# Optimization experiments

Measured on AMD Instinct MI355X. Metric: run time of the kernel, lower is better.

The kernel has to match this reference:

```python
import jax, jax.numpy as jnp
import numpy as np

B, S, D = 8, 2048, 1024  # batch, seq_len, emb_dim == qkv_dim
NEG = -999999.0  # module uses -999999 instead of -inf


def setup_inputs() -> dict:
    key = jax.random.key(0)
    ks = jax.random.split(key, 4)
    inputs = jax.random.normal(ks[0], (B, S, D), dtype=jnp.float32)
    # causal mask, flax attention layout [B, 1, S, S]
    causal = jnp.tril(jnp.ones((S, S), dtype=bool))
    mask = jnp.broadcast_to(causal, (B, 1, S, S))
    scale = 1.0 / np.sqrt(D)
    Wq = jax.random.normal(ks[1], (D, D), dtype=jnp.float32) * scale
    Wk = jax.random.normal(ks[2], (D, D), dtype=jnp.float32) * scale
    Wv = jax.random.normal(ks[3], (D, D), dtype=jnp.float32) * scale
    z = jnp.zeros((D,), dtype=jnp.float32)
    return {"inputs": inputs, "mask": mask, "Wq": Wq, "bq": z, "Wk": Wk,
            "bk": z, "Wv": Wv, "bv": z}


def reference(inputs, mask, Wq, bq, Wk, bk, Wv, bv):
    q = inputs @ Wq + bq  # [B,S,D]
    k = inputs @ Wk + bk
    v = inputs @ Wv + bv
    depth = q.shape[-1]
    q = q / jnp.sqrt(jnp.asarray(depth, q.dtype))
    attn = jnp.einsum('bqd,bkd->bqk', q, k)  # [B,S,S]
    attn = jnp.where(jnp.squeeze(mask, axis=1), attn, NEG)
    attn = jax.nn.softmax(attn, axis=-1)
    return attn @ v  # [B,S,D]
```

## Files before the change

kernel.cpp:

```cpp
#include <hip/hip_runtime.h>
#include <hip/hip_bf16.h>
#include <cstdint>

#define S_LEN 2048
#define D_DIM 1024
#define NB 8

typedef __attribute__((ext_vector_type(8))) short bf16x8;
typedef __attribute__((ext_vector_type(4))) float f32x4;

__device__ __forceinline__ unsigned short f2bf(float f) {
  union { float f; unsigned u; } x; x.f = f;
  unsigned r = x.u + 0x7fffu + ((x.u >> 16) & 1u);
  return (unsigned short)(r >> 16);
}
__device__ __forceinline__ void gload16(const void* g, void* l) {
  __builtin_amdgcn_global_load_lds((const __attribute__((address_space(1))) void*)g,
                                   (__attribute__((address_space(3))) void*)l, 16, 0, 0);
}

__global__ __launch_bounds__(256)
void cvt_f32_bf16(const float* __restrict__ in, unsigned short* __restrict__ out, int n4) {
  int i = blockIdx.x * blockDim.x + threadIdx.x;
  if (i >= n4) return;
  float4 v = reinterpret_cast<const float4*>(in)[i];
  ushort4 o;
  o.x = f2bf(v.x); o.y = f2bf(v.y); o.z = f2bf(v.z); o.w = f2bf(v.w);
  reinterpret_cast<ushort4*>(out)[i] = o;
}

__global__ __launch_bounds__(256)
void transpose_f32_bf16(const float* __restrict__ in, unsigned short* __restrict__ out,
                        int rows, int cols) {
  __shared__ unsigned short tile[32][33];
  int bx = blockIdx.x * 32, by = blockIdx.y * 32;
  int tx = threadIdx.x, ty = threadIdx.y;
  #pragma unroll
  for (int i = ty; i < 32; i += 8)
    tile[i][tx] = f2bf(in[(size_t)(by + i) * cols + bx + tx]);
  __syncthreads();
  #pragma unroll
  for (int i = ty; i < 32; i += 8)
    out[(size_t)(bx + i) * rows + by + tx] = tile[tx][i];
}

__global__ __launch_bounds__(256)
void transpose_bf16(const unsigned short* __restrict__ in, unsigned short* __restrict__ out,
                    int ldin, int ldout, long zin, long zout) {
  __shared__ unsigned short tile[32][33];
  const unsigned short* ip = in + (size_t)blockIdx.z * zin;
  unsigned short* op = out + (size_t)blockIdx.z * zout;
  int bx = blockIdx.x * 32, by = blockIdx.y * 32;
  int tx = threadIdx.x, ty = threadIdx.y;
  #pragma unroll
  for (int i = ty; i < 32; i += 8)
    tile[i][tx] = ip[(size_t)(by + i) * ldin + bx + tx];
  __syncthreads();
  #pragma unroll
  for (int i = ty; i < 32; i += 8)
    op[(size_t)(bx + i) * ldout + by + tx] = tile[tx][i];
}

template<int MODE>
__global__ __launch_bounds__(512, 2)
void gemm8(const unsigned short* __restrict__ Aall, const unsigned short* __restrict__ Btall,
           void* __restrict__ Call, int Kd, int lda, int ldb, int ldc,
           long sAz, long sBz, long sCz,
           const float* __restrict__ b0, const float* __restrict__ b1,
           const float* __restrict__ b2, float* __restrict__ rowsum, int ntn) {
  __shared__ __align__(16) unsigned short As[2][2][8192];
  __shared__ __align__(16) unsigned short Bs[2][2][8192];
  int nwg = gridDim.x, bid = blockIdx.x;
  int wg = (bid & 7) * (nwg >> 3) + (bid >> 3);
  int tm = wg / ntn, tn = wg % ntn;
  int z = blockIdx.z;
  if (MODE == 1 && tn > tm) return;
  const unsigned short* A  = Aall  + (size_t)z * sAz;
  const unsigned short* Bt = Btall + (size_t)z * sBz;
  int m0 = tm * 256, n0 = tn * 256;
  int t = threadIdx.x, lane = t & 63, w = t >> 6;
  int wr = w >> 2, wc = w & 3;
  int lr = lane & 15, lq = lane >> 4;
  int nkt = (MODE == 2) ? (tm + 1) * 4 : (Kd >> 6);

  int offA[8], offB[4];
  #pragma unroll
  for (int mi = 0; mi < 8; ++mi) {
    int row = wr * 128 + mi * 16 + lr;
    offA[mi] = row * 32 + ((lq ^ ((row >> 1) & 3)) * 8);
  }
  #pragma unroll
  for (int ni = 0; ni < 4; ++ni) {
    int row = wc * 64 + ni * 16 + lr;
    offB[ni] = row * 32 + ((lq ^ ((row >> 1) & 3)) * 8);
  }
  int srow[2], soff[2];
  #pragma unroll
  for (int c = 0; c < 2; ++c) {
    int r = c * 128 + w * 16 + (lane >> 2);
    srow[c] = r;
    soff[c] = ((lane & 3) ^ ((r >> 1) & 3)) * 8;
  }

  f32x4 acc[8][4];
  f32x4 zero4 = {0.f, 0.f, 0.f, 0.f};
  #pragma unroll
  for (int mi = 0; mi < 8; ++mi)
    #pragma unroll
    for (int ni = 0; ni < 4; ++ni) acc[mi][ni] = zero4;

  auto stgA = [&](int buf, int kh, int kt) {
    int kb = kt * 64 + kh * 32;
    #pragma unroll
    for (int c = 0; c < 2; ++c)
      gload16(A + (size_t)(m0 + srow[c]) * lda + kb + soff[c],
              &As[buf][kh][c * 4096 + w * 512]);
  };
  auto stgB = [&](int buf, int kh, int kt) {
    int kb = kt * 64 + kh * 32;
    #pragma unroll
    for (int c = 0; c < 2; ++c)
      gload16(Bt + (size_t)(n0 + srow[c]) * ldb + kb + soff[c],
              &Bs[buf][kh][c * 4096 + w * 512]);
  };

  stgA(0, 0, 0); stgB(0, 0, 0); stgA(0, 1, 0); stgB(0, 1, 0);

  int cur = 0;
  for (int kt = 0; kt < nkt; ++kt) {
    bool pf = (kt + 1 < nkt);
    #pragma unroll
    for (int ph = 0; ph < 4; ++ph) {
      const int kk = ph >> 1, mh = ph & 1;
      if (pf || ph < 2) asm volatile("s_waitcnt vmcnt(4)" ::: "memory");
      else              asm volatile("s_waitcnt vmcnt(0)" ::: "memory");
      __builtin_amdgcn_s_barrier();
      __builtin_amdgcn_sched_barrier(0);
      bf16x8 af[4], bfv[4];
      #pragma unroll
      for (int i = 0; i < 4; ++i)
        af[i] = *reinterpret_cast<const bf16x8*>(&As[cur][kk][offA[mh * 4 + i]]);
      #pragma unroll
      for (int i = 0; i < 4; ++i)
        bfv[i] = *reinterpret_cast<const bf16x8*>(&Bs[cur][kk][offB[i]]);
      if (pf) {
        if (ph == 0)      stgA(cur ^ 1, 0, kt + 1);
        else if (ph == 1) stgB(cur ^ 1, 0, kt + 1);
        else if (ph == 2) stgA(cur ^ 1, 1, kt + 1);
        else              stgB(cur ^ 1, 1, kt + 1);
      }
      asm volatile("s_waitcnt lgkmcnt(0)" ::: "memory");
      __builtin_amdgcn_sched_barrier(0);
      __builtin_amdgcn_s_setprio(1);
      #pragma unroll
      for (int i = 0; i < 4; ++i)
        #pragma unroll
        for (int j = 0; j < 4; ++j)
          acc[mh * 4 + i][j] =
              __builtin_amdgcn_mfma_f32_16x16x32_bf16(af[i], bfv[j], acc[mh * 4 + i][j], 0, 0, 0);
      __builtin_amdgcn_s_setprio(0);
    }
    cur ^= 1;
  }

  if (MODE == 0) {
    unsigned short* C = (unsigned short*)Call;
    #pragma unroll
    for (int ni = 0; ni < 4; ++ni) {
      int col = n0 + wc * 64 + ni * 16 + lr;
      float bb, sc;
      if (col < 1024)      { bb = b0[col];        sc = 0.03125f; }
      else if (col < 2048) { bb = b1[col - 1024]; sc = 1.0f; }
      else                 { bb = b2[col - 2048]; sc = 1.0f; }
      #pragma unroll
      for (int mi = 0; mi < 8; ++mi)
        #pragma unroll
        for (int j = 0; j < 4; ++j) {
          int row = m0 + wr * 128 + mi * 16 + lq * 4 + j;
          C[(size_t)row * ldc + col] = f2bf((acc[mi][ni][j] + bb) * sc);
        }
    }
  } else if (MODE == 1) {
    unsigned short* C = (unsigned short*)Call + (size_t)z * sCz;
    float* rs = rowsum + z * S_LEN;
    #pragma unroll
    for (int mi = 0; mi < 8; ++mi)
      #pragma unroll
      for (int j = 0; j < 4; ++j) {
        int row = m0 + wr * 128 + mi * 16 + lq * 4 + j;
        float partial = 0.f;
        #pragma unroll
        for (int ni = 0; ni < 4; ++ni) {
          int col = n0 + wc * 64 + ni * 16 + lr;
          float e = (col <= row) ? __expf(acc[mi][ni][j]) : 0.f;
          partial += e;
          C[(size_t)row * ldc + col] = f2bf(e);
        }
        #pragma unroll
        for (int off = 1; off < 16; off <<= 1) partial += __shfl_xor(partial, off);
        if (lr == 0) atomicAdd(&rs[row], partial);
      }
  } else {
    float* C = (float*)Call + (size_t)z * sCz;
    const float* rs = rowsum + z * S_LEN;
    #pragma unroll
    for (int mi = 0; mi < 8; ++mi)
      #pragma unroll
      for (int j = 0; j < 4; ++j) {
        int row = m0 + wr * 128 + mi * 16 + lq * 4 + j;
        float inv = 1.f / rs[row];
        #pragma unroll
        for (int ni = 0; ni < 4; ++ni) {
          int col = n0 + wc * 64 + ni * 16 + lr;
          C[(size_t)row * ldc + col] = acc[mi][ni][j] * inv;
        }
      }
  }
}

extern "C" void kernel_launch(void* const* d_in, const int* in_sizes, int n_in,
                              void* d_out, int out_size, void* d_ws, size_t ws_size,
                              hipStream_t stream) {
  (void)in_sizes; (void)n_in; (void)out_size; (void)ws_size;
  const float* X  = (const float*)d_in[0];
  const float* Wq = (const float*)d_in[2];
  const float* bq = (const float*)d_in[3];
  const float* Wk = (const float*)d_in[4];
  const float* bk = (const float*)d_in[5];
  const float* Wv = (const float*)d_in[6];
  const float* bv = (const float*)d_in[7];

  char* ws = (char*)d_ws;
  unsigned short* Xb  = (unsigned short*)(ws);
  unsigned short* Wt  = (unsigned short*)(ws + 33554432L);
  float*          Rs  = (float*)(ws + 33554432L);
  unsigned short* QKV = (unsigned short*)(ws + 39845888L);
  unsigned short* Pb  = (unsigned short*)(ws + 140509184L);
  unsigned short* Vt  = Xb;

  cvt_f32_bf16<<<16384, 256, 0, stream>>>(X, Xb, (NB * S_LEN * D_DIM) / 4);
  dim3 tb(32, 8);
  transpose_f32_bf16<<<dim3(32, 32), tb, 0, stream>>>(Wq, Wt + 0L * 1048576L, D_DIM, D_DIM);
  transpose_f32_bf16<<<dim3(32, 32), tb, 0, stream>>>(Wk, Wt + 1L * 1048576L, D_DIM, D_DIM);
  transpose_f32_bf16<<<dim3(32, 32), tb, 0, stream>>>(Wv, Wt + 2L * 1048576L, D_DIM, D_DIM);
  gemm8<0><<<dim3(64 * 12, 1, 1), 512, 0, stream>>>(Xb, Wt, (void*)QKV,
      D_DIM, D_DIM, D_DIM, 3 * D_DIM,
      0L, 0L, 0L, bq, bk, bv, nullptr, 12);
  hipMemsetAsync(Rs, 0, NB * S_LEN * sizeof(float), stream);
  gemm8<1><<<dim3(64, 1, NB), 512, 0, stream>>>(QKV, QKV + 1024, (void*)Pb,
      D_DIM, 3 * D_DIM, 3 * D_DIM, S_LEN,
      (long)S_LEN * 3 * D_DIM, (long)S_LEN * 3 * D_DIM, (long)S_LEN * S_LEN,
      nullptr, nullptr, nullptr, Rs, 8);
  transpose_bf16<<<dim3(32, 64, NB), tb, 0, stream>>>(QKV + 2048, Vt,
      3 * D_DIM, S_LEN, (long)S_LEN * 3 * D_DIM, (long)D_DIM * S_LEN);
  gemm8<2><<<dim3(32, 1, NB), 512, 0, stream>>>(Pb, Vt, d_out,
      S_LEN, S_LEN, S_LEN, D_DIM,
      (long)S_LEN * S_LEN, (long)D_DIM * S_LEN, (long)S_LEN * D_DIM,
      nullptr, nullptr, nullptr, Rs, 4);
}
```

Before: 328.7 us.

## Use 4-stage LDS ring with register double-buffered fragments and staged bf16 stores

```diff
diff --git a/kernel.cpp b/kernel.cpp
--- a/kernel.cpp
+++ b/kernel.cpp
@@ -61,6 +61,20 @@
     op[(size_t)(bx + i) * ldout + by + tx] = tile[tx][i];
 }
 
+#define LDFRAG(S, BUF, MH)                                                        \
+  { _Pragma("unroll") for (int i_ = 0; i_ < 4; ++i_)                              \
+      af##S[i_] = *reinterpret_cast<const bf16x8*>(&As[BUF][offA[(MH)*4+i_]]);    \
+    _Pragma("unroll") for (int i_ = 0; i_ < 4; ++i_)                              \
+      bf##S[i_] = *reinterpret_cast<const bf16x8*>(&Bs[BUF][offB[i_]]); }
+
+#define DOMFMA(S, MH)                                                             \
+  { __builtin_amdgcn_s_setprio(1);                                                \
+    _Pragma("unroll") for (int i_ = 0; i_ < 4; ++i_)                              \
+      _Pragma("unroll") for (int j_ = 0; j_ < 4; ++j_)                            \
+        acc[(MH)*4+i_][j_] = __builtin_amdgcn_mfma_f32_16x16x32_bf16(             \
+            af##S[i_], bf##S[j_], acc[(MH)*4+i_][j_], 0, 0, 0);                   \
+    __builtin_amdgcn_s_setprio(0); }
+
 template<int MODE>
 __global__ __launch_bounds__(512, 2)
 void gemm8(const unsigned short* __restrict__ Aall, const unsigned short* __restrict__ Btall,
@@ -68,8 +82,8 @@
            long sAz, long sBz, long sCz,
            const float* __restrict__ b0, const float* __restrict__ b1,
            const float* __restrict__ b2, float* __restrict__ rowsum, int ntn) {
-  __shared__ __align__(16) unsigned short As[2][2][8192];
-  __shared__ __align__(16) unsigned short Bs[2][2][8192];
+  __shared__ __align__(16) unsigned short As[4][8192];
+  __shared__ __align__(16) unsigned short Bs[4][8192];
   int nwg = gridDim.x, bid = blockIdx.x;
   int wg = (bid & 7) * (nwg >> 3) + (bid >> 3);
   int tm = wg / ntn, tn = wg % ntn;
@@ -81,7 +95,7 @@
   int t = threadIdx.x, lane = t & 63, w = t >> 6;
   int wr = w >> 2, wc = w & 3;
   int lr = lane & 15, lq = lane >> 4;
-  int nkt = (MODE == 2) ? (tm + 1) * 4 : (Kd >> 6);
+  int nkt = (MODE == 2) ? (tm + 1) * 8 : (Kd >> 5);
 
   int offA[8], offB[4];
   #pragma unroll
@@ -109,97 +123,120 @@
     #pragma unroll
     for (int ni = 0; ni < 4; ++ni) acc[mi][ni] = zero4;
 
-  auto stgA = [&](int buf, int kh, int kt) {
-    int kb = kt * 64 + kh * 32;
+  auto stgA = [&](int buf, int kt2) {
+    int kb = kt2 * 32;
     #pragma unroll
     for (int c = 0; c < 2; ++c)
-      gload16(A + (size_t)(m0 + srow[c]) * lda + kb + soff[c],
-              &As[buf][kh][c * 4096 + w * 512]);
+      gload16(A + (size_t)(m0 + srow[c]) * lda + kb + soff[c], &As[buf][c * 4096 + w * 512]);
   };
-  auto stgB = [&](int buf, int kh, int kt) {
-    int kb = kt * 64 + kh * 32;
+  auto stgB = [&](int buf, int kt2) {
+    int kb = kt2 * 32;
     #pragma unroll
     for (int c = 0; c < 2; ++c)
-      gload16(Bt + (size_t)(n0 + srow[c]) * ldb + kb + soff[c],
-              &Bs[buf][kh][c * 4096 + w * 512]);
+      gload16(Bt + (size_t)(n0 + srow[c]) * ldb + kb + soff[c], &Bs[buf][c * 4096 + w * 512]);
   };
 
-  stgA(0, 0, 0); stgB(0, 0, 0); stgA(0, 1, 0); stgB(0, 1, 0);
-
-  int cur = 0;
+  stgA(0, 0); stgB(0, 0); stgA(1, 1); stgB(1, 1); stgA(2, 2); stgB(2, 2);
+  asm volatile("s_waitcnt vmcnt(8)" ::: "memory");
+  __builtin_amdgcn_s_barrier();
+  __builtin_amdgcn_sched_barrier(0);
+  bf16x8 af0[4], bf0[4], af1[4], bf1[4];
+  LDFRAG(0, 0, 0);
+
   for (int kt = 0; kt < nkt; ++kt) {
-    bool pf = (kt + 1 < nkt);
-    #pragma unroll
-    for (int ph = 0; ph < 4; ++ph) {
-      const int kk = ph >> 1, mh = ph & 1;
-      if (pf || ph < 2) asm volatile("s_waitcnt vmcnt(4)" ::: "memory");
-      else              asm volatile("s_waitcnt vmcnt(0)" ::: "memory");
+    int bcur = kt & 3, bpre = (kt + 3) & 3, bnxt = (kt + 1) & 3;
+    bool stg = (kt + 3 < nkt);
+    if (stg) stgA(bpre, kt + 3);
+    LDFRAG(1, bcur, 1);
+    asm volatile("s_waitcnt lgkmcnt(8)" ::: "memory");
+    __builtin_amdgcn_sched_barrier(0);
+    DOMFMA(0, 0);
+    if (stg) stgB(bpre, kt + 3);
+    if (kt + 1 < nkt) {
+      if (kt <= nkt - 4)      asm volatile("s_waitcnt vmcnt(8)" ::: "memory");
+      else if (kt == nkt - 3) asm volatile("s_waitcnt vmcnt(4)" ::: "memory");
+      else                    asm volatile("s_waitcnt vmcnt(0)" ::: "memory");
       __builtin_amdgcn_s_barrier();
       __builtin_amdgcn_sched_barrier(0);
-      bf16x8 af[4], bfv[4];
-      #pragma unroll
-      for (int i = 0; i < 4; ++i)
-        af[i] = *reinterpret_cast<const bf16x8*>(&As[cur][kk][offA[mh * 4 + i]]);
-      #pragma unroll
-      for (int i = 0; i < 4; ++i)
-        bfv[i] = *reinterpret_cast<const bf16x8*>(&Bs[cur][kk][offB[i]]);
-      if (pf) {
-        if (ph == 0)      stgA(cur ^ 1, 0, kt + 1);
-        else if (ph == 1) stgB(cur ^ 1, 0, kt + 1);
-        else if (ph == 2) stgA(cur ^ 1, 1, kt + 1);
-        else              stgB(cur ^ 1, 1, kt + 1);
+      LDFRAG(0, bnxt, 0);
+      asm volatile("s_waitcnt lgkmcnt(8)" ::: "memory");
+    } else {
+      asm volatile("s_waitcnt lgkmcnt(0)" ::: "memory");
+    }
+    __builtin_amdgcn_sched_barrier(0);
+    DOMFMA(1, 1);
+  }
+  __syncthreads();
+
+  unsigned short* ep = &As[0][0] + w * 4096;
+  int lq4 = lq << 4;
+
+  if (MODE == 0) {
+    unsigned short* C = (unsigned short*)Call;
+    #pragma unroll
+    for (int mh = 0; mh < 2; ++mh) {
+      #pragma unroll
+      for (int mi2 = 0; mi2 < 4; ++mi2)
+        #pragma unroll
+        for (int ni = 0; ni < 4; ++ni) {
+          int col = ni * 16 + lr;
+          int gcol = n0 + wc * 64 + col;
+          float bb, sc;
+          if (gcol < 1024)      { bb = b0[gcol];        sc = 0.03125f; }
+          else if (gcol < 2048) { bb = b1[gcol - 1024]; sc = 1.0f; }
+          else                  { bb = b2[gcol - 2048]; sc = 1.0f; }
+          #pragma unroll
+          for (int j = 0; j < 4; ++j) {
+            int lrow = mi2 * 16 + lq * 4 + j;
+            ep[lrow * 64 + (col ^ lq4)] = f2bf((acc[mh * 4 + mi2][ni][j] + bb) * sc);
+          }
+        }
+      #pragma unroll
+      for (int pass = 0; pass < 8; ++pass) {
+        int rrow = pass * 8 + (lane >> 3);
+        int c8 = (lane & 7) * 8;
+        int sw = ((rrow >> 2) & 3) << 4;
+        bf16x8 vv = *reinterpret_cast<const bf16x8*>(&ep[rrow * 64 + (c8 ^ sw)]);
+        int grow = m0 + wr * 128 + mh * 64 + rrow;
+        *reinterpret_cast<bf16x8*>(&C[(size_t)grow * ldc + n0 + wc * 64 + c8]) = vv;
       }
       asm volatile("s_waitcnt lgkmcnt(0)" ::: "memory");
-      __builtin_amdgcn_sched_barrier(0);
-      __builtin_amdgcn_s_setprio(1);
-      #pragma unroll
-      for (int i = 0; i < 4; ++i)
-        #pragma unroll
-        for (int j = 0; j < 4; ++j)
-          acc[mh * 4 + i][j] =
-              __builtin_amdgcn_mfma_f32_16x16x32_bf16(af[i], bfv[j], acc[mh * 4 + i][j], 0, 0, 0);
-      __builtin_amdgcn_s_setprio(0);
-    }
-    cur ^= 1;
-  }
-
-  if (MODE == 0) {
-    unsigned short* C = (unsigned short*)Call;
-    #pragma unroll
-    for (int ni = 0; ni < 4; ++ni) {
-      int col = n0 + wc * 64 + ni * 16 + lr;
-      float bb, sc;
-      if (col < 1024)      { bb = b0[col];        sc = 0.03125f; }
-      else if (col < 2048) { bb = b1[col - 1024]; sc = 1.0f; }
-      else                 { bb = b2[col - 2048]; sc = 1.0f; }
-      #pragma unroll
-      for (int mi = 0; mi < 8; ++mi)
-        #pragma unroll
-        for (int j = 0; j < 4; ++j) {
-          int row = m0 + wr * 128 + mi * 16 + lq * 4 + j;
-          C[(size_t)row * ldc + col] = f2bf((acc[mi][ni][j] + bb) * sc);
-        }
     }
   } else if (MODE == 1) {
     unsigned short* C = (unsigned short*)Call + (size_t)z * sCz;
     float* rs = rowsum + z * S_LEN;
     #pragma unroll
-    for (int mi = 0; mi < 8; ++mi)
-      #pragma unroll
-      for (int j = 0; j < 4; ++j) {
-        int row = m0 + wr * 128 + mi * 16 + lq * 4 + j;
-        float partial = 0.f;
+    for (int mh = 0; mh < 2; ++mh) {
+      #pragma unroll
+      for (int mi2 = 0; mi2 < 4; ++mi2)
         #pragma unroll
-        for (int ni = 0; ni < 4; ++ni) {
-          int col = n0 + wc * 64 + ni * 16 + lr;
-          float e = (col <= row) ? __expf(acc[mi][ni][j]) : 0.f;
-          partial += e;
-          C[(size_t)row * ldc + col] = f2bf(e);
+        for (int j = 0; j < 4; ++j) {
+          int lrow = mi2 * 16 + lq * 4 + j;
+          int grow = m0 + wr * 128 + mh * 64 + lrow;
+          float partial = 0.f;
+          #pragma unroll
+          for (int ni = 0; ni < 4; ++ni) {
+            int col = ni * 16 + lr;
+            int gcol = n0 + wc * 64 + col;
+            float e = (gcol <= grow) ? __expf(acc[mh * 4 + mi2][ni][j]) : 0.f;
+            partial += e;
+            ep[lrow * 64 + (col ^ lq4)] = f2bf(e);
+          }
+          #pragma unroll
+          for (int off = 1; off < 16; off <<= 1) partial += __shfl_xor(partial, off);
+          if (lr == 0) atomicAdd(&rs[grow], partial);
         }
-        #pragma unroll
-        for (int off = 1; off < 16; off <<= 1) partial += __shfl_xor(partial, off);
-        if (lr == 0) atomicAdd(&rs[row], partial);
+      #pragma unroll
+      for (int pass = 0; pass < 8; ++pass) {
+        int rrow = pass * 8 + (lane >> 3);
+        int c8 = (lane & 7) * 8;
+        int sw = ((rrow >> 2) & 3) << 4;
+        bf16x8 vv = *reinterpret_cast<const bf16x8*>(&ep[rrow * 64 + (c8 ^ sw)]);
+        int grow = m0 + wr * 128 + mh * 64 + rrow;
+        *reinterpret_cast<bf16x8*>(&C[(size_t)grow * ldc + n0 + wc * 64 + c8]) = vv;
       }
+      asm volatile("s_waitcnt lgkmcnt(0)" ::: "memory");
+    }
   } else {
     float* C = (float*)Call + (size_t)z * sCz;
     const float* rs = rowsum + z * S_LEN;
```

After: 340.1 us. 3.5% more time.
